# Optimization experiments

Measured on AMD Instinct MI355X. Metric: run time of the kernel, lower is better.

Reference implementation:

```python
import jax, jax.numpy as jnp
import numpy as np

EPS = 1e-05  # config.norm_eps
C = 4        # len('qkvm')

def setup_inputs() -> dict:
    key = jax.random.key(0)
    k1, k2, k3 = jax.random.split(key, 3)
    B, T, D = 4, 4096, 4096
    L_TOT = 48  # (lidx+2)*C with lidx=10
    x = jax.random.normal(k1, (B, T, D), dtype=jnp.float32)
    # torch Linear weights are [out_features, in_features]
    W1 = jax.random.normal(k2, (L_TOT, D), dtype=jnp.float32) * (D ** -0.5)
    W2 = jax.random.normal(k3, (L_TOT, L_TOT), dtype=jnp.float32) * (L_TOT ** -0.5)
    return {"x": x, "W1": W1, "W2": W2}

def reference(x, W1, W2):
    # RMSNorm without scale
    var = jnp.mean(x * x, axis=-1, keepdims=True)
    xn = x * jax.lax.rsqrt(var + EPS)                      # [B, T, D]
    h = jnp.einsum('btd,ld->btl', xn, W1)                  # [B, T, l]
    dw = jnp.einsum('btk,lk->btl', jax.nn.gelu(h, approximate=False), W2)
    B, T, Ltot = dw.shape
    # rearrange 'B T (C L) -> C B T L'
    return jnp.transpose(dw.reshape(B, T, C, Ltot // C), (2, 0, 1, 3))
```

## Files before the change

kernel.cpp:

```cpp
#include <hip/hip_runtime.h>
#include <hip/hip_bf16.h>

#define DDIM 4096
#define LTOT 48

typedef __attribute__((ext_vector_type(4))) float f32x4;
typedef __attribute__((ext_vector_type(8))) short bf16x8;

__device__ __forceinline__ void gload_lds16(const void* g, void* l) {
    __builtin_amdgcn_global_load_lds(
        (const __attribute__((address_space(1))) void*)g,
        (__attribute__((address_space(3))) void*)l, 16, 0, 0);
}

__device__ __forceinline__ unsigned cvt_pk(float x, float y) {
    union { __hip_bfloat162 h; unsigned u; } c;
    c.h = __float22bfloat162_rn(make_float2(x, y));
    return c.u;
}

__global__ void w1cvt_kernel(const float* __restrict__ w1, ushort* __restrict__ w1b) {
    int i = blockIdx.x * 256 + threadIdx.x;
    union { float f; unsigned u; } v; v.f = w1[i];
    unsigned r = v.u + 0x7fffu + ((v.u >> 16) & 1u);
    w1b[i] = (ushort)(r >> 16);
}

__global__ __launch_bounds__(256, 4) void fused_kernel(
        const float* __restrict__ x,
        const ushort* __restrict__ w1b,
        const float* __restrict__ w2,
        float* __restrict__ out) {
    __shared__ __align__(1024) char smem[32768];
    __shared__ float ssw[4][16];
    __shared__ float scl[16];

    const int tid  = threadIdx.x;
    const int wave = tid >> 6;
    const int lane = tid & 63;
    const int rl   = lane & 15;
    const int kg   = lane >> 4;
    const int row0 = blockIdx.x * 16;
    const int kw   = wave * 1024;
    const int rot  = blockIdx.x & 15;

    char* wbase = smem + wave * 8192;

    int dso[2][2];
    #pragma unroll
    for (int h = 0; h < 2; ++h)
        #pragma unroll
        for (int p = 0; p < 2; ++p)
            dso[h][p] = rl * 256 + (((h * 8 + kg * 2 + p) ^ rl) << 4);

    auto stage = [&](int t) {
        const int kb = kw + ((t + rot) & 15) * 64;
        char* lb = wbase + (t & 1) * 4096;
        #pragma unroll
        for (int i = 0; i < 4; ++i) {
            int rloc = i * 4 + kg;
            int blkg = rl ^ rloc;
            const float* src = x + (size_t)(row0 + rloc) * DDIM + kb + blkg * 4;
            gload_lds16(src, lb + i * 1024);
        }
    };

    auto loadB = [&](int s, bf16x8 (&bl)[6]) {
        const ushort* bp = w1b + (size_t)rl * DDIM + kw + ((s + rot) & 15) * 64 + kg * 8;
        #pragma unroll
        for (int n = 0; n < 3; ++n)
            #pragma unroll
            for (int h = 0; h < 2; ++h)
                bl[n * 2 + h] = *(const bf16x8*)(bp + n * 16 * DDIM + h * 32);
    };

    float ss = 0.f;
    f32x4 acc[3] = {{0.f,0.f,0.f,0.f},{0.f,0.f,0.f,0.f},{0.f,0.f,0.f,0.f}};
    bf16x8 bA[6], bB[6];

    stage(0); stage(1); loadB(0, bA);

    auto body = [&](int s, bf16x8 (&bu)[6], bf16x8 (&bl)[6]) {
        asm volatile("s_waitcnt vmcnt(4)" ::: "memory");
        char* lb = wbase + (s & 1) * 4096;
        f32x4 a[2][2];
        #pragma unroll
        for (int h = 0; h < 2; ++h)
            #pragma unroll
            for (int p = 0; p < 2; ++p)
                a[h][p] = *(const f32x4*)(lb + dso[h][p]);
        if (s < 15) loadB(s + 1, bl);
        #pragma unroll
        for (int h = 0; h < 2; ++h) {
            f32x4 a0 = a[h][0], a1 = a[h][1];
            ss = fmaf(a0.x, a0.x, ss); ss = fmaf(a0.y, a0.y, ss);
            ss = fmaf(a0.z, a0.z, ss); ss = fmaf(a0.w, a0.w, ss);
            ss = fmaf(a1.x, a1.x, ss); ss = fmaf(a1.y, a1.y, ss);
            ss = fmaf(a1.z, a1.z, ss); ss = fmaf(a1.w, a1.w, ss);
            union { bf16x8 v; unsigned u[4]; } af;
            af.u[0] = cvt_pk(a0.x, a0.y); af.u[1] = cvt_pk(a0.z, a0.w);
            af.u[2] = cvt_pk(a1.x, a1.y); af.u[3] = cvt_pk(a1.z, a1.w);
            #pragma unroll
            for (int n = 0; n < 3; ++n)
                acc[n] = __builtin_amdgcn_mfma_f32_16x16x32_bf16(
                             af.v, bu[n * 2 + h], acc[n], 0, 0, 0);
        }
        asm volatile("s_waitcnt lgkmcnt(0)" ::: "memory");
        if (s < 14) stage(s + 2);
    };

    for (int sp = 0; sp < 8; ++sp) {
        body(2 * sp,     bA, bB);
        body(2 * sp + 1, bB, bA);
    }

    ss += __shfl_xor(ss, 16);
    ss += __shfl_xor(ss, 32);
    if (lane < 16) ssw[wave][lane] = ss;
    __syncthreads();

    float* dots = (float*)smem;
    float* gbuf = (float*)(smem + 12288);
    float* w2s  = (float*)(smem + 15360);

    #pragma unroll
    for (int n = 0; n < 3; ++n)
        #pragma unroll
        for (int i = 0; i < 4; ++i)
            dots[(wave * 16 + kg * 4 + i) * 48 + n * 16 + rl] = acc[n][i];
    for (int i = tid; i < LTOT * LTOT; i += 256) w2s[i] = w2[i];
    __syncthreads();

    if (tid < 16) {
        float st = ssw[0][tid] + ssw[1][tid] + ssw[2][tid] + ssw[3][tid];
        scl[tid] = rsqrtf(st * (1.0f / (float)DDIM) + 1e-5f);
    }
    __syncthreads();

    #pragma unroll
    for (int i = 0; i < 3; ++i) {
        int v = tid + i * 256;
        int row = v / 48, col = v - row * 48;
        float d = dots[(0 * 16 + row) * 48 + col] + dots[(1 * 16 + row) * 48 + col]
                + dots[(2 * 16 + row) * 48 + col] + dots[(3 * 16 + row) * 48 + col];
        float h = d * scl[row];
        gbuf[row * 48 + col] = h * 0.5f * (1.0f + erff(h * 0.70710678118654752f));
    }
    __syncthreads();

    #pragma unroll
    for (int i = 0; i < 3; ++i) {
        int v = tid + i * 256;
        int row = v / 48, l = v - row * 48;
        float sacc = 0.f;
        #pragma unroll
        for (int k = 0; k < LTOT; ++k)
            sacc = fmaf(gbuf[row * 48 + k], w2s[l * LTOT + k], sacc);
        int rg = row0 + row;
        int b  = rg >> 12;
        int t  = rg & 4095;
        int c  = l / 12, j = l - c * 12;
        out[(((size_t)(c * 4 + b) * 4096 + t) * 12) + j] = sacc;
    }
}

extern "C" void kernel_launch(void* const* d_in, const int* in_sizes, int n_in,
                              void* d_out, int out_size, void* d_ws, size_t ws_size,
                              hipStream_t stream) {
    const float* x  = (const float*)d_in[0];
    const float* W1 = (const float*)d_in[1];
    const float* W2 = (const float*)d_in[2];
    float* out = (float*)d_out;
    ushort* w1b = (ushort*)d_ws;

    w1cvt_kernel<<<(LTOT * DDIM) / 256, 256, 0, stream>>>(W1, w1b);
    fused_kernel<<<16384 / 16, 256, 0, stream>>>(x, w1b, W2, out);
}
```

Baseline: 69.91 us.

## Process 32 rows per block to reuse W1 fragments across two MFMA tiles

```diff
diff --git a/kernel.cpp b/kernel.cpp
--- a/kernel.cpp
+++ b/kernel.cpp
@@ -26,41 +26,43 @@
     w1b[i] = (ushort)(r >> 16);
 }
 
-__global__ __launch_bounds__(256, 4) void fused_kernel(
+__global__ __launch_bounds__(256, 2) void fused_kernel(
         const float* __restrict__ x,
         const ushort* __restrict__ w1b,
         const float* __restrict__ w2,
         float* __restrict__ out) {
-    __shared__ __align__(1024) char smem[32768];
-    __shared__ float ssw[4][16];
-    __shared__ float scl[16];
+    __shared__ __align__(1024) char smem[65536];
+    __shared__ float ssw[4][32];
+    __shared__ float scl[32];
 
     const int tid  = threadIdx.x;
     const int wave = tid >> 6;
     const int lane = tid & 63;
     const int rl   = lane & 15;
     const int kg   = lane >> 4;
-    const int row0 = blockIdx.x * 16;
+    const int row0 = blockIdx.x * 32;
     const int kw   = wave * 1024;
     const int rot  = blockIdx.x & 15;
 
-    char* wbase = smem + wave * 8192;
+    char* wbase = smem + wave * 16384;
 
-    int dso[2][2];
+    int dso[2][2][2];
     #pragma unroll
-    for (int h = 0; h < 2; ++h)
+    for (int T = 0; T < 2; ++T)
         #pragma unroll
-        for (int p = 0; p < 2; ++p)
-            dso[h][p] = rl * 256 + (((h * 8 + kg * 2 + p) ^ rl) << 4);
+        for (int h = 0; h < 2; ++h)
+            #pragma unroll
+            for (int p = 0; p < 2; ++p)
+                dso[T][h][p] = (T * 16 + rl) * 256 + (((h * 8 + kg * 2 + p) ^ rl) << 4);
 
     auto stage = [&](int t) {
         const int kb = kw + ((t + rot) & 15) * 64;
-        char* lb = wbase + (t & 1) * 4096;
+        char* lb = wbase + (t & 1) * 8192;
         #pragma unroll
-        for (int i = 0; i < 4; ++i) {
-            int rloc = i * 4 + kg;
-            int blkg = rl ^ rloc;
-            const float* src = x + (size_t)(row0 + rloc) * DDIM + kb + blkg * 4;
+        for (int i = 0; i < 8; ++i) {
+            int r    = i * 4 + kg;
+            int blkg = rl ^ (r & 15);
+            const float* src = x + (size_t)(row0 + r) * DDIM + kb + blkg * 4;
             gload_lds16(src, lb + i * 1024);
         }
     };
@@ -74,36 +76,51 @@
                 bl[n * 2 + h] = *(const bf16x8*)(bp + n * 16 * DDIM + h * 32);
     };
 
-    float ss = 0.f;
-    f32x4 acc[3] = {{0.f,0.f,0.f,0.f},{0.f,0.f,0.f,0.f},{0.f,0.f,0.f,0.f}};
+    float ss0 = 0.f, ss1 = 0.f;
+    f32x4 acc0[3] = {{0.f,0.f,0.f,0.f},{0.f,0.f,0.f,0.f},{0.f,0.f,0.f,0.f}};
+    f32x4 acc1[3] = {{0.f,0.f,0.f,0.f},{0.f,0.f,0.f,0.f},{0.f,0.f,0.f,0.f}};
     bf16x8 bA[6], bB[6];
 
-    stage(0); stage(1); loadB(0, bA);
+    stage(0); loadB(0, bA); stage(1);
 
     auto body = [&](int s, bf16x8 (&bu)[6], bf16x8 (&bl)[6]) {
-        asm volatile("s_waitcnt vmcnt(4)" ::: "memory");
-        char* lb = wbase + (s & 1) * 4096;
-        f32x4 a[2][2];
+        if (s == 0)       asm volatile("s_waitcnt vmcnt(14)" ::: "memory");
+        else if (s == 15) asm volatile("s_waitcnt vmcnt(6)"  ::: "memory");
+        else              asm volatile("s_waitcnt vmcnt(8)"  ::: "memory");
+        char* lb = wbase + (s & 1) * 8192;
+        f32x4 a[2][2][2];
         #pragma unroll
-        for (int h = 0; h < 2; ++h)
+        for (int T = 0; T < 2; ++T)
             #pragma unroll
-            for (int p = 0; p < 2; ++p)
-                a[h][p] = *(const f32x4*)(lb + dso[h][p]);
+            for (int h = 0; h < 2; ++h)
+                #pragma unroll
+                for (int p = 0; p < 2; ++p)
+                    a[T][h][p] = *(const f32x4*)(lb + dso[T][h][p]);
         if (s < 15) loadB(s + 1, bl);
         #pragma unroll
         for (int h = 0; h < 2; ++h) {
-            f32x4 a0 = a[h][0], a1 = a[h][1];
-            ss = fmaf(a0.x, a0.x, ss); ss = fmaf(a0.y, a0.y, ss);
-            ss = fmaf(a0.z, a0.z, ss); ss = fmaf(a0.w, a0.w, ss);
-            ss = fmaf(a1.x, a1.x, ss); ss = fmaf(a1.y, a1.y, ss);
-            ss = fmaf(a1.z, a1.z, ss); ss = fmaf(a1.w, a1.w, ss);
-            union { bf16x8 v; unsigned u[4]; } af;
+            f32x4 a0 = a[0][h][0], a1 = a[0][h][1];
+            f32x4 c0 = a[1][h][0], c1 = a[1][h][1];
+            ss0 = fmaf(a0.x, a0.x, ss0); ss0 = fmaf(a0.y, a0.y, ss0);
+            ss0 = fmaf(a0.z, a0.z, ss0); ss0 = fmaf(a0.w, a0.w, ss0);
+            ss0 = fmaf(a1.x, a1.x, ss0); ss0 = fmaf(a1.y, a1.y, ss0);
+            ss0 = fmaf(a1.z, a1.z, ss0); ss0 = fmaf(a1.w, a1.w, ss0);
+            ss1 = fmaf(c0.x, c0.x, ss1); ss1 = fmaf(c0.y, c0.y, ss1);
+            ss1 = fmaf(c0.z, c0.z, ss1); ss1 = fmaf(c0.w, c0.w, ss1);
+            ss1 = fmaf(c1.x, c1.x, ss1); ss1 = fmaf(c1.y, c1.y, ss1);
+            ss1 = fmaf(c1.z, c1.z, ss1); ss1 = fmaf(c1.w, c1.w, ss1);
+            union { bf16x8 v; unsigned u[4]; } af, ag;
             af.u[0] = cvt_pk(a0.x, a0.y); af.u[1] = cvt_pk(a0.z, a0.w);
             af.u[2] = cvt_pk(a1.x, a1.y); af.u[3] = cvt_pk(a1.z, a1.w);
+            ag.u[0] = cvt_pk(c0.x, c0.y); ag.u[1] = cvt_pk(c0.z, c0.w);
+            ag.u[2] = cvt_pk(c1.x, c1.y); ag.u[3] = cvt_pk(c1.z, c1.w);
             #pragma unroll
-            for (int n = 0; n < 3; ++n)
-                acc[n] = __builtin_amdgcn_mfma_f32_16x16x32_bf16(
-                             af.v, bu[n * 2 + h], acc[n], 0, 0, 0);
+            for (int n = 0; n < 3; ++n) {
+                acc0[n] = __builtin_amdgcn_mfma_f32_16x16x32_bf16(
+                              af.v, bu[n * 2 + h], acc0[n], 0, 0, 0);
+                acc1[n] = __builtin_amdgcn_mfma_f32_16x16x32_bf16(
+                              ag.v, bu[n * 2 + h], acc1[n], 0, 0, 0);
+            }
         }
         asm volatile("s_waitcnt lgkmcnt(0)" ::: "memory");
         if (s < 14) stage(s + 2);
@@ -114,42 +131,44 @@
         body(2 * sp + 1, bB, bA);
     }
 
-    ss += __shfl_xor(ss, 16);
-    ss += __shfl_xor(ss, 32);
-    if (lane < 16) ssw[wave][lane] = ss;
+    ss0 += __shfl_xor(ss0, 16); ss0 += __shfl_xor(ss0, 32);
+    ss1 += __shfl_xor(ss1, 16); ss1 += __shfl_xor(ss1, 32);
+    if (lane < 16) { ssw[wave][lane] = ss0; ssw[wave][16 + lane] = ss1; }
+
+    asm volatile("s_waitcnt vmcnt(0) lgkmcnt(0)" ::: "memory");
     __syncthreads();
 
     float* dots = (float*)smem;
-    float* gbuf = (float*)(smem + 12288);
-    float* w2s  = (float*)(smem + 15360);
+    float* gbuf = (float*)(smem + 24576);
+    float* w2s  = (float*)(smem + 30720);
 
     #pragma unroll
     for (int n = 0; n < 3; ++n)
         #pragma unroll
-        for (int i = 0; i < 4; ++i)
-            dots[(wave * 16 + kg * 4 + i) * 48 + n * 16 + rl] = acc[n][i];
+        for (int i = 0; i < 4; ++i) {
+            dots[(wave * 32 + kg * 4 + i) * 48 + n * 16 + rl]      = acc0[n][i];
+            dots[(wave * 32 + 16 + kg * 4 + i) * 48 + n * 16 + rl] = acc1[n][i];
+        }
     for (int i = tid; i < LTOT * LTOT; i += 256) w2s[i] = w2[i];
-    __syncthreads();
-
-    if (tid < 16) {
+    if (tid < 32) {
         float st = ssw[0][tid] + ssw[1][tid] + ssw[2][tid] + ssw[3][tid];
         scl[tid] = rsqrtf(st * (1.0f / (float)DDIM) + 1e-5f);
     }
     __syncthreads();
 
     #pragma unroll
-    for (int i = 0; i < 3; ++i) {
+    for (int i = 0; i < 6; ++i) {
         int v = tid + i * 256;
         int row = v / 48, col = v - row * 48;
-        float d = dots[(0 * 16 + row) * 48 + col] + dots[(1 * 16 + row) * 48 + col]
-                + dots[(2 * 16 + row) * 48 + col] + dots[(3 * 16 + row) * 48 + col];
+        float d = dots[(0 * 32 + row) * 48 + col] + dots[(1 * 32 + row) * 48 + col]
+                + dots[(2 * 32 + row) * 48 + col] + dots[(3 * 32 + row) * 48 + col];
         float h = d * scl[row];
         gbuf[row * 48 + col] = h * 0.5f * (1.0f + erff(h * 0.70710678118654752f));
     }
     __syncthreads();
 
     #pragma unroll
-    for (int i = 0; i < 3; ++i) {
+    for (int i = 0; i < 6; ++i) {
         int v = tid + i * 256;
         int row = v / 48, l = v - row * 48;
         float sacc = 0.f;
@@ -174,5 +193,5 @@
     ushort* w1b = (ushort*)d_ws;
 
     w1cvt_kernel<<<(LTOT * DDIM) / 256, 256, 0, stream>>>(W1, w1b);
-    fused_kernel<<<16384 / 16, 256, 0, stream>>>(x, w1b, W2, out);
+    fused_kernel<<<16384 / 32, 256, 0, stream>>>(x, w1b, W2, out);
 }
```

Result: faster. 58.07 us (median of 2 runs) (-16.9%).

## Process 64 rows per block to reuse W1 fragments across four row tiles

Applied to the files above, without the earlier changes.

```diff
diff --git a/kernel.cpp b/kernel.cpp
--- a/kernel.cpp
+++ b/kernel.cpp
@@ -26,41 +26,43 @@
     w1b[i] = (ushort)(r >> 16);
 }
 
-__global__ __launch_bounds__(256, 4) void fused_kernel(
+__global__ __launch_bounds__(256, 1) void fused_kernel(
         const float* __restrict__ x,
         const ushort* __restrict__ w1b,
         const float* __restrict__ w2,
         float* __restrict__ out) {
-    __shared__ __align__(1024) char smem[32768];
-    __shared__ float ssw[4][16];
-    __shared__ float scl[16];
+    __shared__ __align__(1024) char smem[131072];
+    __shared__ float ssw[4][64];
+    __shared__ float scl[64];
 
     const int tid  = threadIdx.x;
     const int wave = tid >> 6;
     const int lane = tid & 63;
     const int rl   = lane & 15;
     const int kg   = lane >> 4;
-    const int row0 = blockIdx.x * 16;
+    const int row0 = blockIdx.x * 64;
     const int kw   = wave * 1024;
     const int rot  = blockIdx.x & 15;
 
-    char* wbase = smem + wave * 8192;
+    char* wbase = smem + wave * 32768;
 
-    int dso[2][2];
+    int dso[4][2][2];
     #pragma unroll
-    for (int h = 0; h < 2; ++h)
+    for (int T = 0; T < 4; ++T)
         #pragma unroll
-        for (int p = 0; p < 2; ++p)
-            dso[h][p] = rl * 256 + (((h * 8 + kg * 2 + p) ^ rl) << 4);
+        for (int h = 0; h < 2; ++h)
+            #pragma unroll
+            for (int p = 0; p < 2; ++p)
+                dso[T][h][p] = (T * 16 + rl) * 256 + (((h * 8 + kg * 2 + p) ^ rl) << 4);
 
     auto stage = [&](int t) {
         const int kb = kw + ((t + rot) & 15) * 64;
-        char* lb = wbase + (t & 1) * 4096;
+        char* lb = wbase + (t & 1) * 16384;
         #pragma unroll
-        for (int i = 0; i < 4; ++i) {
-            int rloc = i * 4 + kg;
-            int blkg = rl ^ rloc;
-            const float* src = x + (size_t)(row0 + rloc) * DDIM + kb + blkg * 4;
+        for (int i = 0; i < 16; ++i) {
+            int r    = i * 4 + kg;
+            int blkg = rl ^ (r & 15);
+            const float* src = x + (size_t)(row0 + r) * DDIM + kb + blkg * 4;
             gload_lds16(src, lb + i * 1024);
         }
     };
@@ -74,36 +76,47 @@
                 bl[n * 2 + h] = *(const bf16x8*)(bp + n * 16 * DDIM + h * 32);
     };
 
-    float ss = 0.f;
-    f32x4 acc[3] = {{0.f,0.f,0.f,0.f},{0.f,0.f,0.f,0.f},{0.f,0.f,0.f,0.f}};
+    float ss[4] = {0.f, 0.f, 0.f, 0.f};
+    f32x4 acc[4][3];
+    #pragma unroll
+    for (int T = 0; T < 4; ++T)
+        #pragma unroll
+        for (int n = 0; n < 3; ++n)
+            acc[T][n] = (f32x4){0.f, 0.f, 0.f, 0.f};
     bf16x8 bA[6], bB[6];
 
-    stage(0); stage(1); loadB(0, bA);
+    stage(0); loadB(0, bA); stage(1);
 
     auto body = [&](int s, bf16x8 (&bu)[6], bf16x8 (&bl)[6]) {
-        asm volatile("s_waitcnt vmcnt(4)" ::: "memory");
-        char* lb = wbase + (s & 1) * 4096;
-        f32x4 a[2][2];
+        if (s == 0)       asm volatile("s_waitcnt vmcnt(22)" ::: "memory");
+        else if (s == 15) asm volatile("s_waitcnt vmcnt(6)"  ::: "memory");
+        else              asm volatile("s_waitcnt vmcnt(16)" ::: "memory");
+        char* lb = wbase + (s & 1) * 16384;
+        if (s < 15) loadB(s + 1, bl);
+
         #pragma unroll
-        for (int h = 0; h < 2; ++h)
+        for (int T = 0; T < 4; ++T) {
+            f32x4 a[2][2];
             #pragma unroll
-            for (int p = 0; p < 2; ++p)
-                a[h][p] = *(const f32x4*)(lb + dso[h][p]);
-        if (s < 15) loadB(s + 1, bl);
-        #pragma unroll
-        for (int h = 0; h < 2; ++h) {
-            f32x4 a0 = a[h][0], a1 = a[h][1];
-            ss = fmaf(a0.x, a0.x, ss); ss = fmaf(a0.y, a0.y, ss);
-            ss = fmaf(a0.z, a0.z, ss); ss = fmaf(a0.w, a0.w, ss);
-            ss = fmaf(a1.x, a1.x, ss); ss = fmaf(a1.y, a1.y, ss);
-            ss = fmaf(a1.z, a1.z, ss); ss = fmaf(a1.w, a1.w, ss);
-            union { bf16x8 v; unsigned u[4]; } af;
-            af.u[0] = cvt_pk(a0.x, a0.y); af.u[1] = cvt_pk(a0.z, a0.w);
-            af.u[2] = cvt_pk(a1.x, a1.y); af.u[3] = cvt_pk(a1.z, a1.w);
+            for (int h = 0; h < 2; ++h)
+                #pragma unroll
+                for (int p = 0; p < 2; ++p)
+                    a[h][p] = *(const f32x4*)(lb + dso[T][h][p]);
             #pragma unroll
-            for (int n = 0; n < 3; ++n)
-                acc[n] = __builtin_amdgcn_mfma_f32_16x16x32_bf16(
-                             af.v, bu[n * 2 + h], acc[n], 0, 0, 0);
+            for (int h = 0; h < 2; ++h) {
+                f32x4 a0 = a[h][0], a1 = a[h][1];
+                ss[T] = fmaf(a0.x, a0.x, ss[T]); ss[T] = fmaf(a0.y, a0.y, ss[T]);
+                ss[T] = fmaf(a0.z, a0.z, ss[T]); ss[T] = fmaf(a0.w, a0.w, ss[T]);
+                ss[T] = fmaf(a1.x, a1.x, ss[T]); ss[T] = fmaf(a1.y, a1.y, ss[T]);
+                ss[T] = fmaf(a1.z, a1.z, ss[T]); ss[T] = fmaf(a1.w, a1.w, ss[T]);
+                union { bf16x8 v; unsigned u[4]; } af;
+                af.u[0] = cvt_pk(a0.x, a0.y); af.u[1] = cvt_pk(a0.z, a0.w);
+                af.u[2] = cvt_pk(a1.x, a1.y); af.u[3] = cvt_pk(a1.z, a1.w);
+                #pragma unroll
+                for (int n = 0; n < 3; ++n)
+                    acc[T][n] = __builtin_amdgcn_mfma_f32_16x16x32_bf16(
+                                    af.v, bu[n * 2 + h], acc[T][n], 0, 0, 0);
+            }
         }
         asm volatile("s_waitcnt lgkmcnt(0)" ::: "memory");
         if (s < 14) stage(s + 2);
@@ -114,42 +127,48 @@
         body(2 * sp + 1, bB, bA);
     }
 
-    ss += __shfl_xor(ss, 16);
-    ss += __shfl_xor(ss, 32);
-    if (lane < 16) ssw[wave][lane] = ss;
+    #pragma unroll
+    for (int T = 0; T < 4; ++T) {
+        float v = ss[T];
+        v += __shfl_xor(v, 16);
+        v += __shfl_xor(v, 32);
+        if (lane < 16) ssw[wave][T * 16 + lane] = v;
+    }
+
+    asm volatile("s_waitcnt vmcnt(0) lgkmcnt(0)" ::: "memory");
     __syncthreads();
 
     float* dots = (float*)smem;
-    float* gbuf = (float*)(smem + 12288);
-    float* w2s  = (float*)(smem + 15360);
+    float* gbuf = (float*)(smem + 49152);
+    float* w2s  = (float*)(smem + 61440);
 
     #pragma unroll
-    for (int n = 0; n < 3; ++n)
+    for (int T = 0; T < 4; ++T)
         #pragma unroll
-        for (int i = 0; i < 4; ++i)
-            dots[(wave * 16 + kg * 4 + i) * 48 + n * 16 + rl] = acc[n][i];
+        for (int n = 0; n < 3; ++n)
+            #pragma unroll
+            for (int i = 0; i < 4; ++i)
+                dots[(wave * 64 + T * 16 + kg * 4 + i) * 48 + n * 16 + rl] = acc[T][n][i];
     for (int i = tid; i < LTOT * LTOT; i += 256) w2s[i] = w2[i];
-    __syncthreads();
-
-    if (tid < 16) {
+    if (tid < 64) {
         float st = ssw[0][tid] + ssw[1][tid] + ssw[2][tid] + ssw[3][tid];
         scl[tid] = rsqrtf(st * (1.0f / (float)DDIM) + 1e-5f);
     }
     __syncthreads();
 
     #pragma unroll
-    for (int i = 0; i < 3; ++i) {
+    for (int i = 0; i < 12; ++i) {
         int v = tid + i * 256;
         int row = v / 48, col = v - row * 48;
-        float d = dots[(0 * 16 + row) * 48 + col] + dots[(1 * 16 + row) * 48 + col]
-                + dots[(2 * 16 + row) * 48 + col] + dots[(3 * 16 + row) * 48 + col];
+        float d = dots[(0 * 64 + row) * 48 + col] + dots[(1 * 64 + row) * 48 + col]
+                + dots[(2 * 64 + row) * 48 + col] + dots[(3 * 64 + row) * 48 + col];
         float h = d * scl[row];
         gbuf[row * 48 + col] = h * 0.5f * (1.0f + erff(h * 0.70710678118654752f));
     }
     __syncthreads();
 
     #pragma unroll
-    for (int i = 0; i < 3; ++i) {
+    for (int i = 0; i < 12; ++i) {
         int v = tid + i * 256;
         int row = v / 48, l = v - row * 48;
         float sacc = 0.f;
@@ -174,5 +193,5 @@
     ushort* w1b = (ushort*)d_ws;
 
     w1cvt_kernel<<<(LTOT * DDIM) / 256, 256, 0, stream>>>(W1, w1b);
-    fused_kernel<<<16384 / 16, 256, 0, stream>>>(x, w1b, W2, out);
+    fused_kernel<<<16384 / 64, 256, 0, stream>>>(x, w1b, W2, out);
 }
```

After: 61.18 us. -12.5%, faster.
